# Kernel tuning notes

Measured on AMD Instinct MI355X. Metric: run time of the kernel, lower is better.

The kernel has to match this reference:

```python
import jax, jax.numpy as jnp
import numpy as np

B, C, H, W = 4, 3, 32, 32
N_IMAGES = 32
TIMESTEPS = 20


def _extract_patches(x, pad_mode):
    """3x3 patches at every spatial location. x: [B,C,H,W] -> [B,C,9,H,W]."""
    if pad_mode == 'wrap':
        xp = jnp.pad(x, ((0, 0), (0, 0), (1, 1), (1, 1)), mode='wrap')
    else:
        xp = jnp.pad(x, ((0, 0), (0, 0), (1, 1), (1, 1)))
    h, w = x.shape[2], x.shape[3]
    sl = [xp[:, :, di:di + h, dj:dj + w] for di in range(3) for dj in range(3)]
    return jnp.stack(sl, axis=2)  # [B,C,9,H,W], k = di*3+dj (torch unfold order)


def setup_inputs() -> dict:
    key = jax.random.key(0)
    k1, k2 = jax.random.split(key)
    x = jax.random.normal(k1, (B, C, H, W), dtype=jnp.float32)
    images = jax.random.uniform(k2, (N_IMAGES, C, H, W), dtype=jnp.float32)
    # linear beta schedule, as in _noise_buffers
    betas = jnp.linspace(1e-4, 0.02, TIMESTEPS, dtype=jnp.float32)
    alpha_cumprod = jnp.cumprod(1.0 - betas)
    mu_sched = jnp.sqrt(alpha_cumprod)
    sigma_sched = jnp.sqrt(1.0 - alpha_cumprod)
    return {"x": x, "images": images, "mu_sched": mu_sched,
            "sigma_sched": sigma_sched, "t": 10}


def reference(x, images, mu_sched, sigma_sched, t):
    mu = mu_sched[t]
    sigma = sigma_sched[t]
    b, c, h, w = x.shape

    # x-side: circular-padded 3x3 patches and their squared norms
    xp = _extract_patches(x, 'wrap').reshape(b, c * 9, h, w)   # [B,C*9,H,W]
    x_norms = jnp.sum(xp * xp, axis=1)                          # [B,H,W]

    # dataset-side: zero-padded 3x3 patches at every pixel of every image
    ip = _extract_patches(images, 'zeros')                      # [N,C,9,H,W]
    patches = ip.transpose(0, 3, 4, 1, 2).reshape(-1, c * 9)    # [P, C*9], P=N*H*W
    pnorms = jnp.sum(patches * patches, axis=1)                 # [P]
    pcenters = patches.reshape(-1, c, 9)[:, :, 4]               # [P,C] center pixel (1,1)

    # conv2d(x_pad, patches) == contraction over the C*9 patch axis
    conv = jnp.einsum('bkhw,pk->bphw', xp, patches)             # [B,P,H,W]

    inv2s2 = 1.0 / (2.0 * sigma * sigma)
    log_w = -(x_norms[:, None] - 2.0 * mu * conv
              + (mu * mu) * pnorms[None, :, None, None]) * inv2s2  # [B,P,H,W]

    # stable softmax-style weights over the patch axis (== online LSE result)
    m = jnp.max(log_w, axis=1)                                  # [B,H,W]
    wgt = jnp.exp(log_w - m[:, None])                           # [B,P,H,W]
    sum_w = jnp.sum(wgt, axis=1)                                # [B,H,W]

    # sum_p w * (x - mu * pcenter) = x*sum_w - mu * (w @ pcenters)
    wc = jnp.einsum('bphw,pc->bchw', wgt, pcenters)             # [B,C,H,W]
    sum_wd = x * sum_w[:, None] - mu * wc
    return -sum_wd / (sigma * sigma * sum_w[:, None])
```

## Files before the change

kernel.cpp:

```cpp
#include <hip/hip_runtime.h>
#include <cstddef>

#define P_TOTAL 32768
#define Q_TOTAL 4096
#define NSPLIT 128
#define KPS 256
#define TILES 16
#define NGROUP 8
#define QPERWG 256
#define NQG (Q_TOTAL / QPERWG)
#define GRID (NSPLIT * NQG)

#define KEYS_B 16384
#define VT_OFF KEYS_B
#define VT_PITCH 528
#define VT_ZERO (VT_OFF + 4 * VT_PITCH)
#define P_OFF (VT_OFF + 2624)
#define P_FRAG 1280
#define P_WAVE (4 * P_FRAG)
#define LDS_TOTAL (P_OFF + 4 * P_WAVE)

typedef _Float16 half8 __attribute__((ext_vector_type(8)));
typedef __fp16 fp16x2 __attribute__((ext_vector_type(2)));
typedef __fp16 fp16x4 __attribute__((ext_vector_type(4)));
typedef float floatx4 __attribute__((ext_vector_type(4)));

__device__ __forceinline__ float fexp2(float x) {
#if defined(__has_builtin) && __has_builtin(__builtin_amdgcn_exp2f)
    return __builtin_amdgcn_exp2f(x);
#else
    return exp2f(x);
#endif
}

__global__ __launch_bounds__(256) void qbuild_k(
    const float* __restrict__ x, _Float16* __restrict__ q16)
{
    int q = blockIdx.x * 256 + threadIdx.x;
    int b = q >> 10, rem = q & 1023, h = rem >> 5, w = rem & 31;
    const float* xb = x + (size_t)b * 3072;
    _Float16 row[32];
    #pragma unroll
    for (int c = 0; c < 3; c++)
      #pragma unroll
      for (int di = 0; di < 3; di++)
        #pragma unroll
        for (int dj = 0; dj < 3; dj++)
            row[c * 9 + di * 3 + dj] =
                (_Float16)xb[c * 1024 + ((h + di + 31) & 31) * 32 + ((w + dj + 31) & 31)];
    row[27] = (_Float16)1.0f;
    row[28] = (_Float16)0.f; row[29] = (_Float16)0.f;
    row[30] = (_Float16)0.f; row[31] = (_Float16)0.f;
    _Float16* qp = q16 + (size_t)q * 32;
    #pragma unroll
    for (int u = 0; u < 4; u++) ((float4*)qp)[u] = ((float4*)row)[u];
}

__global__ __launch_bounds__(256) void score_k(
    const _Float16* __restrict__ q16, const float* __restrict__ images,
    const float* __restrict__ mu_sched, const float* __restrict__ sigma_sched,
    const int* __restrict__ tptr, float* __restrict__ partials)
{
    __shared__ char lds[LDS_TOTAL];
    int tid = threadIdx.x;
    int split = blockIdx.x >> 4;
    int qg    = blockIdx.x & 15;

    int t = tptr[0];
    float mu = mu_sched[t], sg = sigma_sched[t];
    const float LOG2E = 1.4426950408889634f;
    float inv2s2 = 1.0f / (2.0f * sg * sg);
    float s1     = 2.0f * mu * inv2s2 * LOG2E;
    float bscale = -mu * mu * inv2s2 * LOG2E;

    {
        int r = tid;
        int p = split * KPS + r;
        int n = p >> 10, rem = p & 1023, i = rem >> 5, j = rem & 31;
        const float* img = images + (size_t)n * 3072;
        _Float16 hrow[32];
        float pnorm = 0.f, c0 = 0.f, c1 = 0.f, c2 = 0.f;
        #pragma unroll
        for (int c = 0; c < 3; c++)
          #pragma unroll
          for (int di = 0; di < 3; di++)
            #pragma unroll
            for (int dj = 0; dj < 3; dj++) {
                int ii = i + di - 1, jj = j + dj - 1;
                float val = 0.f;
                if (ii >= 0 && ii < 32 && jj >= 0 && jj < 32)
                    val = img[c * 1024 + ii * 32 + jj];
                hrow[c * 9 + di * 3 + dj] = (_Float16)(val * s1);
                pnorm = fmaf(val, val, pnorm);
                if (di == 1 && dj == 1) { if (c == 0) c0 = val; else if (c == 1) c1 = val; else c2 = val; }
            }
        hrow[27] = (_Float16)(pnorm * bscale);
        hrow[28] = (_Float16)0.f; hrow[29] = (_Float16)0.f;
        hrow[30] = (_Float16)0.f; hrow[31] = (_Float16)0.f;
        int sw = (r >> 1) & 3;
        float4* src4 = (float4*)hrow;
        #pragma unroll
        for (int c = 0; c < 4; c++)
            *(float4*)(lds + r * 64 + ((c ^ sw) << 4)) = src4[c];
        _Float16* vt = (_Float16*)(lds + VT_OFF);
        vt[0 * (VT_PITCH / 2) + r] = (_Float16)1.0f;
        vt[1 * (VT_PITCH / 2) + r] = (_Float16)c0;
        vt[2 * (VT_PITCH / 2) + r] = (_Float16)c1;
        vt[3 * (VT_PITCH / 2) + r] = (_Float16)c2;
        if (tid < 128) ((float*)(lds + VT_ZERO))[tid] = 0.f;
    }

    int lane = tid & 63, wid = tid >> 6;
    int col  = lane & 15, quad = lane >> 4;
    int qbase = qg * QPERWG + wid * 64;

    half8 qf[4];
    #pragma unroll
    for (int f = 0; f < 4; f++)
        qf[f] = *(const half8*)(q16 + (size_t)(qbase + f * 16 + col) * 32 + quad * 8);
    __syncthreads();

    int swc = (col >> 1) & 3;
    const char* abase = lds + col * 64 + ((quad ^ swc) << 4);

    float mx[4];
    {
        floatx4 mv[4];
        #pragma unroll
        for (int f = 0; f < 4; f++) mv[f] = (floatx4){-3e38f, -3e38f, -3e38f, -3e38f};
        #pragma unroll 4
        for (int tile = 0; tile < TILES; tile++) {
            half8 ak = *(const half8*)(abase + tile * 1024);
            #pragma unroll
            for (int f = 0; f < 4; f++) {
                floatx4 a = __builtin_amdgcn_mfma_f32_16x16x32_f16(
                    ak, qf[f], (floatx4){0.f, 0.f, 0.f, 0.f}, 0, 0, 0);
                mv[f] = __builtin_elementwise_max(mv[f], a);
            }
        }
        #pragma unroll
        for (int f = 0; f < 4; f++) {
            mx[f] = fmaxf(fmaxf(mv[f][0], mv[f][1]), fmaxf(mv[f][2], mv[f][3]));
            mx[f] = fmaxf(mx[f], __shfl_xor(mx[f], 16, 64));
            mx[f] = fmaxf(mx[f], __shfl_xor(mx[f], 32, 64));
        }
    }
    floatx4 nmv[4];
    #pragma unroll
    for (int f = 0; f < 4; f++)
        nmv[f] = (floatx4){-mx[f], -mx[f], -mx[f], -mx[f]};

    if (quad == 0) {
        #pragma unroll
        for (int f = 0; f < 4; f++)
            partials[(size_t)split * Q_TOTAL + qbase + f * 16 + col] = mx[f];
    }

    const char* pwave = lds + P_OFF + wid * P_WAVE;
    char* pwbase = (char*)pwave + col * 80 + quad * 8;
    const char* prbase = pwave + col * 80 + quad * 16;
    const char* vbase = lds + VT_OFF + (col < 4 ? col * VT_PITCH : 4 * VT_PITCH)
                        + quad * 16;

    floatx4 acc[4];
    #pragma unroll
    for (int f = 0; f < 4; f++) acc[f] = (floatx4){0.f, 0.f, 0.f, 0.f};

    for (int g = 0; g < NGROUP; g++) {
        half8 ak0 = *(const half8*)(abase + (2 * g) * 1024);
        half8 ak1 = *(const half8*)(abase + (2 * g + 1) * 1024);
        half8 vb  = *(const half8*)(vbase + g * 64);
        #pragma unroll
        for (int f = 0; f < 4; f++) {
            floatx4 a0 = __builtin_amdgcn_mfma_f32_16x16x32_f16(ak0, qf[f], nmv[f], 0, 0, 0);
            floatx4 a1 = __builtin_amdgcn_mfma_f32_16x16x32_f16(ak1, qf[f], nmv[f], 0, 0, 0);
            fp16x2 p00 = __builtin_amdgcn_cvt_pkrtz(fexp2(a0[0]), fexp2(a0[1]));
            fp16x2 p01 = __builtin_amdgcn_cvt_pkrtz(fexp2(a0[2]), fexp2(a0[3]));
            fp16x2 p10 = __builtin_amdgcn_cvt_pkrtz(fexp2(a1[0]), fexp2(a1[1]));
            fp16x2 p11 = __builtin_amdgcn_cvt_pkrtz(fexp2(a1[2]), fexp2(a1[3]));
            fp16x4 w0 = __builtin_shufflevector(p00, p01, 0, 1, 2, 3);
            fp16x4 w1 = __builtin_shufflevector(p10, p11, 0, 1, 2, 3);
            *(fp16x4*)(pwbase + f * P_FRAG)      = w0;
            *(fp16x4*)(pwbase + f * P_FRAG + 32) = w1;
        }
        #pragma unroll
        for (int f = 0; f < 4; f++) {
            half8 pa = *(const half8*)(prbase + f * P_FRAG);
            acc[f] = __builtin_amdgcn_mfma_f32_16x16x32_f16(pa, vb, acc[f], 0, 0, 0);
        }
    }

    if (col < 4) {
        const size_t PL = (size_t)NSPLIT * Q_TOTAL;
        float* plane = partials + (size_t)(col + 1) * PL + (size_t)split * Q_TOTAL;
        #pragma unroll
        for (int f = 0; f < 4; f++)
            #pragma unroll
            for (int r = 0; r < 4; r++)
                plane[qbase + f * 16 + quad * 4 + r] = acc[f][r];
    }
}

__global__ __launch_bounds__(256) void combine_k(
    const float* __restrict__ x, const float* __restrict__ partials,
    const float* __restrict__ mu_sched, const float* __restrict__ sigma_sched,
    const int* __restrict__ tptr, float* __restrict__ out)
{
    int q = blockIdx.x * 256 + threadIdx.x;
    int t = tptr[0];
    float mu = mu_sched[t], sg = sigma_sched[t];
    float inv_s2 = 1.0f / (sg * sg);

    const size_t PL = (size_t)NSPLIT * Q_TOTAL;
    float M = -3e38f, S = 0.f, W0 = 0.f, W1 = 0.f, W2 = 0.f;
    for (int sp = 0; sp < NSPLIT; sp++) {
        size_t idx = (size_t)sp * Q_TOTAL + q;
        float mval = partials[idx];
        float sval = partials[idx + PL];
        float w0v  = partials[idx + PL * 2];
        float w1v  = partials[idx + PL * 3];
        float w2v  = partials[idx + PL * 4];
        float mnew = fmaxf(M, mval);
        float sco = fexp2(M - mnew);
        float scn = fexp2(mval - mnew);
        S  = fmaf(S,  sco, sval * scn);
        W0 = fmaf(W0, sco, w0v * scn);
        W1 = fmaf(W1, sco, w1v * scn);
        W2 = fmaf(W2, sco, w2v * scn);
        M = mnew;
    }
    float invS = 1.0f / S;
    int b = q >> 10, rem = q & 1023;
    #pragma unroll
    for (int c = 0; c < 3; c++) {
        float Wc = (c == 0) ? W0 : (c == 1 ? W1 : W2);
        float xc = x[(size_t)b * 3072 + c * 1024 + rem];
        out[(size_t)b * 3072 + c * 1024 + rem] = -(xc - mu * Wc * invS) * inv_s2;
    }
}

extern "C" void kernel_launch(void* const* d_in, const int* in_sizes, int n_in,
                              void* d_out, int out_size, void* d_ws, size_t ws_size,
                              hipStream_t stream) {
    const float* x      = (const float*)d_in[0];
    const float* images = (const float*)d_in[1];
    const float* mu_s   = (const float*)d_in[2];
    const float* sg_s   = (const float*)d_in[3];
    const int*   tptr   = (const int*)d_in[4];
    float* out = (float*)d_out;

    float*    partials = (float*)d_ws;
    _Float16* q16      = (_Float16*)((char*)d_ws + (size_t)5 * NSPLIT * Q_TOTAL * 4);

    qbuild_k<<<Q_TOTAL / 256, 256, 0, stream>>>(x, q16);
    score_k<<<GRID, 256, 0, stream>>>(q16, images, mu_s, sg_s, tptr, partials);
    combine_k<<<Q_TOTAL / 256, 256, 0, stream>>>(
        x, partials, mu_s, sg_s, tptr, out);
}
```

Measured before the change: 114.0 us.

## Feed exp weights directly from registers into second MFMA, skip LDS round-trip

The patch order is permuted when building the keys so that the fp16 exp weights produced by the score MFMA already sit in the B-operand layout of the weighted-sum MFMA. This removes the per-wave LDS staging buffer and its write/read traffic, swapping the operand roles so the value matrix becomes the A operand. The output now comes from lanes with quad==0, and the combine kernel splits its serial merge over the splits into two independent chains for more parallelism. The risk is that the permutation and the operand mapping must match exactly, and lanes with col>=4 issue MFMAs on zero operands.

```diff
diff --git a/kernel.cpp b/kernel.cpp
--- a/kernel.cpp
+++ b/kernel.cpp
@@ -14,16 +14,15 @@
 #define KEYS_B 16384
 #define VT_OFF KEYS_B
 #define VT_PITCH 528
-#define VT_ZERO (VT_OFF + 4 * VT_PITCH)
-#define P_OFF (VT_OFF + 2624)
-#define P_FRAG 1280
-#define P_WAVE (4 * P_FRAG)
-#define LDS_TOTAL (P_OFF + 4 * P_WAVE)
+#define LDS_TOTAL (VT_OFF + 4 * VT_PITCH)
 
 typedef _Float16 half8 __attribute__((ext_vector_type(8)));
 typedef __fp16 fp16x2 __attribute__((ext_vector_type(2)));
 typedef __fp16 fp16x4 __attribute__((ext_vector_type(4)));
+typedef __fp16 fp16x8 __attribute__((ext_vector_type(8)));
 typedef float floatx4 __attribute__((ext_vector_type(4)));
+
+union h8cast { fp16x8 a; half8 b; };
 
 __device__ __forceinline__ float fexp2(float x) {
 #if defined(__has_builtin) && __has_builtin(__builtin_amdgcn_exp2f)
@@ -75,7 +74,9 @@
 
     {
         int r = tid;
-        int p = split * KPS + r;
+        int m16 = r & 15, tt = (r >> 4) & 1, tp = r >> 5;
+        int kk = tp * 32 + (m16 >> 2) * 8 + tt * 4 + (m16 & 3);
+        int p = split * KPS + kk;
         int n = p >> 10, rem = p & 1023, i = rem >> 5, j = rem & 31;
         const float* img = images + (size_t)n * 3072;
         _Float16 hrow[32];
@@ -103,11 +104,10 @@
         for (int c = 0; c < 4; c++)
             *(float4*)(lds + r * 64 + ((c ^ sw) << 4)) = src4[c];
         _Float16* vt = (_Float16*)(lds + VT_OFF);
-        vt[0 * (VT_PITCH / 2) + r] = (_Float16)1.0f;
-        vt[1 * (VT_PITCH / 2) + r] = (_Float16)c0;
-        vt[2 * (VT_PITCH / 2) + r] = (_Float16)c1;
-        vt[3 * (VT_PITCH / 2) + r] = (_Float16)c2;
-        if (tid < 128) ((float*)(lds + VT_ZERO))[tid] = 0.f;
+        vt[0 * (VT_PITCH / 2) + kk] = (_Float16)1.0f;
+        vt[1 * (VT_PITCH / 2) + kk] = (_Float16)c0;
+        vt[2 * (VT_PITCH / 2) + kk] = (_Float16)c1;
+        vt[3 * (VT_PITCH / 2) + kk] = (_Float16)c2;
     }
 
     int lane = tid & 63, wid = tid >> 6;
@@ -156,20 +156,17 @@
             partials[(size_t)split * Q_TOTAL + qbase + f * 16 + col] = mx[f];
     }
 
-    const char* pwave = lds + P_OFF + wid * P_WAVE;
-    char* pwbase = (char*)pwave + col * 80 + quad * 8;
-    const char* prbase = pwave + col * 80 + quad * 16;
-    const char* vbase = lds + VT_OFF + (col < 4 ? col * VT_PITCH : 4 * VT_PITCH)
-                        + quad * 16;
-
+    const char* vrow = lds + VT_OFF + col * VT_PITCH;
     floatx4 acc[4];
     #pragma unroll
     for (int f = 0; f < 4; f++) acc[f] = (floatx4){0.f, 0.f, 0.f, 0.f};
 
+    #pragma unroll 2
     for (int g = 0; g < NGROUP; g++) {
         half8 ak0 = *(const half8*)(abase + (2 * g) * 1024);
         half8 ak1 = *(const half8*)(abase + (2 * g + 1) * 1024);
-        half8 vb  = *(const half8*)(vbase + g * 64);
+        half8 av = (half8)(_Float16)0.f;
+        if (col < 4) av = *(const half8*)(vrow + g * 64 + quad * 16);
         #pragma unroll
         for (int f = 0; f < 4; f++) {
             floatx4 a0 = __builtin_amdgcn_mfma_f32_16x16x32_f16(ak0, qf[f], nmv[f], 0, 0, 0);
@@ -178,26 +175,23 @@
             fp16x2 p01 = __builtin_amdgcn_cvt_pkrtz(fexp2(a0[2]), fexp2(a0[3]));
             fp16x2 p10 = __builtin_amdgcn_cvt_pkrtz(fexp2(a1[0]), fexp2(a1[1]));
             fp16x2 p11 = __builtin_amdgcn_cvt_pkrtz(fexp2(a1[2]), fexp2(a1[3]));
-            fp16x4 w0 = __builtin_shufflevector(p00, p01, 0, 1, 2, 3);
-            fp16x4 w1 = __builtin_shufflevector(p10, p11, 0, 1, 2, 3);
-            *(fp16x4*)(pwbase + f * P_FRAG)      = w0;
-            *(fp16x4*)(pwbase + f * P_FRAG + 32) = w1;
-        }
+            fp16x4 lo = __builtin_shufflevector(p00, p01, 0, 1, 2, 3);
+            fp16x4 hi = __builtin_shufflevector(p10, p11, 0, 1, 2, 3);
+            h8cast u; u.a = __builtin_shufflevector(lo, hi, 0, 1, 2, 3, 4, 5, 6, 7);
+            acc[f] = __builtin_amdgcn_mfma_f32_16x16x32_f16(av, u.b, acc[f], 0, 0, 0);
+        }
+    }
+
+    if (quad == 0) {
+        const size_t PL = (size_t)NSPLIT * Q_TOTAL;
         #pragma unroll
         for (int f = 0; f < 4; f++) {
-            half8 pa = *(const half8*)(prbase + f * P_FRAG);
-            acc[f] = __builtin_amdgcn_mfma_f32_16x16x32_f16(pa, vb, acc[f], 0, 0, 0);
-        }
-    }
-
-    if (col < 4) {
-        const size_t PL = (size_t)NSPLIT * Q_TOTAL;
-        float* plane = partials + (size_t)(col + 1) * PL + (size_t)split * Q_TOTAL;
-        #pragma unroll
-        for (int f = 0; f < 4; f++)
-            #pragma unroll
-            for (int r = 0; r < 4; r++)
-                plane[qbase + f * 16 + quad * 4 + r] = acc[f][r];
+            size_t idx = (size_t)split * Q_TOTAL + qbase + f * 16 + col;
+            partials[idx + PL]     = acc[f][0];
+            partials[idx + PL * 2] = acc[f][1];
+            partials[idx + PL * 3] = acc[f][2];
+            partials[idx + PL * 4] = acc[f][3];
+        }
     }
 }
 
@@ -212,23 +206,40 @@
     float inv_s2 = 1.0f / (sg * sg);
 
     const size_t PL = (size_t)NSPLIT * Q_TOTAL;
-    float M = -3e38f, S = 0.f, W0 = 0.f, W1 = 0.f, W2 = 0.f;
-    for (int sp = 0; sp < NSPLIT; sp++) {
-        size_t idx = (size_t)sp * Q_TOTAL + q;
-        float mval = partials[idx];
-        float sval = partials[idx + PL];
-        float w0v  = partials[idx + PL * 2];
-        float w1v  = partials[idx + PL * 3];
-        float w2v  = partials[idx + PL * 4];
-        float mnew = fmaxf(M, mval);
-        float sco = fexp2(M - mnew);
-        float scn = fexp2(mval - mnew);
-        S  = fmaf(S,  sco, sval * scn);
-        W0 = fmaf(W0, sco, w0v * scn);
-        W1 = fmaf(W1, sco, w1v * scn);
-        W2 = fmaf(W2, sco, w2v * scn);
-        M = mnew;
-    }
+    float M1 = -3e38f, S1 = 0.f, A1 = 0.f, B1 = 0.f, C1 = 0.f;
+    float M2 = -3e38f, S2 = 0.f, A2 = 0.f, B2 = 0.f, C2 = 0.f;
+    #pragma unroll 4
+    for (int sp = 0; sp < NSPLIT / 2; sp++) {
+        {
+            size_t idx = (size_t)sp * Q_TOTAL + q;
+            float mval = partials[idx];
+            float mnew = fmaxf(M1, mval);
+            float sco = fexp2(M1 - mnew), scn = fexp2(mval - mnew);
+            S1 = fmaf(S1, sco, partials[idx + PL] * scn);
+            A1 = fmaf(A1, sco, partials[idx + PL * 2] * scn);
+            B1 = fmaf(B1, sco, partials[idx + PL * 3] * scn);
+            C1 = fmaf(C1, sco, partials[idx + PL * 4] * scn);
+            M1 = mnew;
+        }
+        {
+            size_t idx = (size_t)(sp + NSPLIT / 2) * Q_TOTAL + q;
+            float mval = partials[idx];
+            float mnew = fmaxf(M2, mval);
+            float sco = fexp2(M2 - mnew), scn = fexp2(mval - mnew);
+            S2 = fmaf(S2, sco, partials[idx + PL] * scn);
+            A2 = fmaf(A2, sco, partials[idx + PL * 2] * scn);
+            B2 = fmaf(B2, sco, partials[idx + PL * 3] * scn);
+            C2 = fmaf(C2, sco, partials[idx + PL * 4] * scn);
+            M2 = mnew;
+        }
+    }
+    float M = fmaxf(M1, M2);
+    float r1 = fexp2(M1 - M), r2 = fexp2(M2 - M);
+    float S  = S1 * r1 + S2 * r2;
+    float W0 = A1 * r1 + A2 * r2;
+    float W1 = B1 * r1 + B2 * r2;
+    float W2 = C1 * r1 + C2 * r2;
+
     float invS = 1.0f / S;
     int b = q >> 10, rem = q & 1023;
     #pragma unroll
```

New measurement: 110.9 us. 1.03x faster.
